# Optimization experiments

Hardware: AMD Instinct MI355X
Metric: run time of the kernel (lower is better)

Reference implementation:

```python
import jax, jax.numpy as jnp
import numpy as np

C = 512
C8 = C // 8  # reduceRate = 8


def setup_inputs() -> dict:
    key = jax.random.key(0)
    ks = jax.random.split(key, 8)
    B, H, W = 4, 64, 64
    x = jax.random.normal(ks[0], (B, C, H, W), dtype=jnp.float32)
    # 1x1 convs == per-pixel linear maps: weight [out, in], bias [out]
    sb = 1.0 / np.sqrt(C)
    Wb = jax.random.uniform(ks[1], (C8, C), jnp.float32, -sb, sb)
    bb = jax.random.uniform(ks[2], (C8,), jnp.float32, -sb, sb)
    Wc = jax.random.uniform(ks[3], (C8, C), jnp.float32, -sb, sb)
    bc = jax.random.uniform(ks[4], (C8,), jnp.float32, -sb, sb)
    Wd = jax.random.uniform(ks[5], (C, C), jnp.float32, -sb, sb)
    bd = jax.random.uniform(ks[6], (C,), jnp.float32, -sb, sb)
    # nn.Parameter(torch.zeros(1)) -> use small nonzero so grads are nontrivial
    alpha = jnp.full((1,), 0.1, dtype=jnp.float32)
    return {"x": x, "Wb": Wb, "bb": bb, "Wc": Wc, "bc": bc,
            "Wd": Wd, "bd": bd, "alpha": alpha}


def reference(x, Wb, bb, Wc, bc, Wd, bd, alpha):
    B, Cin, H, W = x.shape
    N = H * W
    xf = x.reshape(B, Cin, N)                                    # [B,C,N]
    feat_b = jnp.einsum('oc,bcn->bon', Wb, xf) + bb[None, :, None]  # [B,C/8,N]
    feat_c = jnp.einsum('oc,bcn->bon', Wc, xf) + bc[None, :, None]  # [B,C/8,N]
    # attention_s[b,n,m] = softmax_m( b^T c ), unscaled as in source
    attn = jax.nn.softmax(jnp.einsum('bkn,bkm->bnm', feat_b, feat_c), axis=-1)
    feat_d = jnp.einsum('oc,bcn->bon', Wd, xf) + bd[None, :, None]  # [B,C,N]
    # feat_e = feat_d @ attn^T : e[b,c,n] = sum_m d[b,c,m] * attn[b,n,m]
    feat_e = jnp.einsum('bcm,bnm->bcn', feat_d, attn)
    out = (alpha[0] * feat_e).reshape(B, Cin, H, W) + x
    return out
```

## Files before the change

### kernel.cpp

```cpp
#include <hip/hip_runtime.h>
#include <hip/hip_bf16.h>
#include <math.h>

#define BB 4
#define CC 512
#define NN 4096
#define LOG2E 1.4426950408889634f

typedef short short8 __attribute__((ext_vector_type(8)));
typedef float f32x4 __attribute__((ext_vector_type(4)));
typedef float f32x16 __attribute__((ext_vector_type(16)));
typedef unsigned int u32x2 __attribute__((ext_vector_type(2)));

#define MFMA16(a, b, c) __builtin_amdgcn_mfma_f32_16x16x32_bf16((a), (b), (c), 0, 0, 0)
#define MFMA32(a, b, c) __builtin_amdgcn_mfma_f32_32x32x16_bf16((a), (b), (c), 0, 0, 0)

static __device__ __forceinline__ unsigned short f2bf(float f) {
    union { float f; unsigned int u; } v; v.f = f;
    unsigned int r = v.u + 0x7FFFu + ((v.u >> 16) & 1u);
    return (unsigned short)(r >> 16);
}

static __device__ __forceinline__ unsigned int pk2bf(float a, float b) {
    __hip_bfloat162 t = __float22bfloat162_rn(make_float2(a, b));
    return *(unsigned int*)&t;
}

static __device__ __forceinline__ void gload16(const void* g, void* l) {
    __builtin_amdgcn_global_load_lds(
        (const __attribute__((address_space(1))) unsigned int*)g,
        (__attribute__((address_space(3))) unsigned int*)l, 16, 0, 0);
}

__global__ __launch_bounds__(256) void k_wconv(
    const float* __restrict__ Wb, const float* __restrict__ bb,
    const float* __restrict__ Wc, const float* __restrict__ bc,
    const float* __restrict__ Wd, const float* __restrict__ bd,
    unsigned short* __restrict__ Wcat, float* __restrict__ bcat)
{
    int r = blockIdx.x;
    int t = threadIdx.x;
    const float* src; const float* bsrc; int bi; float scale;
    if (r < 64)       { src = Wb + (size_t)r * 512;         bsrc = bb; bi = r;       scale = LOG2E; }
    else if (r < 128) { src = Wc + (size_t)(r - 64) * 512;  bsrc = bc; bi = r - 64;  scale = 1.0f; }
    else              { src = Wd + (size_t)(r - 128) * 512; bsrc = bd; bi = r - 128; scale = 1.0f; }
    float2 v = *(const float2*)&src[t * 2];
    *(unsigned int*)&Wcat[(size_t)r * 512 + t * 2] = pk2bf(v.x * scale, v.y * scale);
    if (t == 0) bcat[r] = bsrc[bi] * scale;
}

__global__ __launch_bounds__(256) void k_transpose(
    const float* __restrict__ x, unsigned short* __restrict__ xT)
{
    __shared__ float lds[64][65];
    int bid = blockIdx.x;
    int cb = bid & 7;
    int nb = (bid >> 3) & 63;
    int b  = bid >> 9;
    int t = threadIdx.x;
    int r = t >> 4;
    int q = t & 15;

#pragma unroll
    for (int p = 0; p < 4; ++p) {
        int c = p * 16 + r;
        const float4 v = *(const float4*)&x[((size_t)(b * CC + cb * 64 + c)) * NN + nb * 64 + q * 4];
        lds[c][q * 4 + 0] = v.x;
        lds[c][q * 4 + 1] = v.y;
        lds[c][q * 4 + 2] = v.z;
        lds[c][q * 4 + 3] = v.w;
    }
    __syncthreads();
#pragma unroll
    for (int p = 0; p < 4; ++p) {
        int n = p * 16 + r;
        ushort4 o;
        o.x = f2bf(lds[q * 4 + 0][n]);
        o.y = f2bf(lds[q * 4 + 1][n]);
        o.z = f2bf(lds[q * 4 + 2][n]);
        o.w = f2bf(lds[q * 4 + 3][n]);
        *(ushort4*)&xT[((size_t)(b * NN + nb * 64 + n)) * CC + cb * 64 + q * 4] = o;
    }
}

__global__ __launch_bounds__(256) void k_feat(
    const unsigned short* __restrict__ xT,
    const unsigned short* __restrict__ Wcat,
    const float* __restrict__ bcat,
    unsigned short* __restrict__ Q,
    unsigned short* __restrict__ Kf,
    unsigned short* __restrict__ Vtl)
{
    int bid = blockIdx.x;
    int ob = bid % 10;
    int nb = (bid / 10) & 63;
    int b  = bid / 640;
    int t = threadIdx.x, w = t >> 6, lane = t & 63;
    int lr = lane & 15, lg = lane >> 4;

    int o_local = w * 16 + lr;
    int wr = (ob == 0) ? o_local : (ob == 1 ? 64 + o_local : 128 + (ob - 2) * 64 + o_local);
    const unsigned short* Wrow = Wcat + (size_t)wr * CC;
    const unsigned short* xrow = xT + ((size_t)(b * NN + nb * 64)) * CC;

    f32x4 acc[4] = {};

    for (int kt = 0; kt < 8; ++kt) {
        int k0 = kt * 64;
        short8 bfr[2];
#pragma unroll
        for (int ks = 0; ks < 2; ++ks)
            bfr[ks] = *(const short8*)&Wrow[k0 + ks * 32 + lg * 8];
#pragma unroll
        for (int rf = 0; rf < 4; ++rf) {
#pragma unroll
            for (int ks = 0; ks < 2; ++ks) {
                short8 a = *(const short8*)&xrow[(size_t)(rf * 16 + lr) * CC + k0 + ks * 32 + lg * 8];
                acc[rf] = MFMA16(a, bfr[ks], acc[rf]);
            }
        }
    }

    float bias = bcat[wr];
#pragma unroll
    for (int rf = 0; rf < 4; ++rf) {
        if (ob < 2) {
            unsigned short* dst = (ob == 0) ? Q : Kf;
#pragma unroll
            for (int i = 0; i < 4; ++i) {
                int n = nb * 64 + rf * 16 + lg * 4 + i;
                dst[((size_t)(b * NN + n)) * 64 + o_local] = f2bf(acc[rf][i] + bias);
            }
        } else {
            int row = (ob - 2) * 64 + o_local;
            int nl = rf * 16 + lg * 4;
            ushort4 o4;
            o4.x = f2bf(acc[rf][0] + bias);
            o4.y = f2bf(acc[rf][1] + bias);
            o4.z = f2bf(acc[rf][2] + bias);
            o4.w = f2bf(acc[rf][3] + bias);
            *(ushort4*)&Vtl[(((size_t)(b * 64 + nb)) * CC + row) * 64 + nl] = o4;
        }
    }
}

__global__ __launch_bounds__(512, 1) void k_attn(
    const unsigned short* __restrict__ Q,
    const unsigned short* __restrict__ Kf,
    const unsigned short* __restrict__ Vtl,
    const float* __restrict__ x,
    const float* __restrict__ alpha_p,
    float* __restrict__ out)
{
    __shared__ __align__(16) unsigned short Klds[2][64 * 64];
    __shared__ __align__(16) unsigned short Vlds[2][256 * 64];
    __shared__ __align__(16) unsigned short Plds[128 * 64];
    __shared__ float Lacc[2][128];

    int bid0 = blockIdx.x;
    int bid = ((bid0 & 7) << 5) | (bid0 >> 3);
    int cb = bid & 1;
    int qb = (bid >> 1) & 31;
    int b  = bid >> 6;
    int tid = threadIdx.x;
    int w = tid >> 6, lane = tid & 63;
    int l31 = lane & 31, h = lane >> 5;
    int qi = w >> 1, mi = w & 1;

    const char* Kbase = (const char*)Kf + (size_t)b * NN * 128;
    const char* Vbase = (const char*)Vtl + (((size_t)b * 64) * CC + (size_t)cb * 256) * 128;

    short8 qfr[4];
    {
        const unsigned short* qp = Q + ((size_t)(b * NN) + qb * 128 + qi * 32 + l31) * 64;
#pragma unroll
        for (int kk = 0; kk < 4; ++kk)
            qfr[kk] = *(const short8*)&qp[kk * 16 + h * 8];
    }

    int pb[4];
#pragma unroll
    for (int kk = 0; kk < 4; ++kk)
        pb[kk] = (l31 * 128 + kk * 32 + h * 16) ^ ((l31 & 7) << 4);
    int pwa[4];
#pragma unroll
    for (int j = 0; j < 4; ++j)
        pwa[j] = (l31 * 128 + mi * 64 + j * 16 + h * 8) ^ ((l31 & 7) << 4);

#define STAGE(T, BUF)                                                          \
    do {                                                                       \
        const char* ks_ = Kbase + (size_t)(T) * 8192;                          \
        const char* vs_ = Vbase + (size_t)(T) * 65536;                         \
        {                                                                      \
            int du_ = w * 1024;                                                \
            int dl_ = du_ + lane * 16;                                         \
            int sl_ = dl_ ^ (((dl_ >> 7) & 7) << 4);                           \
            gload16(ks_ + sl_, (char*)&Klds[BUF][0] + du_);                    \
        }                                                                      \
        _Pragma("unroll")                                                      \
        for (int i_ = 0; i_ < 4; ++i_) {                                       \
            int du_ = i_ * 8192 + w * 1024;                                    \
            int dl_ = du_ + lane * 16;                                         \
            int sl_ = dl_ ^ (((dl_ >> 7) & 7) << 4);                           \
            gload16(vs_ + sl_, (char*)&Vlds[BUF][0] + du_);                    \
        }                                                                      \
    } while (0)

    f32x16 acc[4] = {};
    float lsum = 0.f;

    STAGE(0, 0);
    asm volatile("s_waitcnt vmcnt(0)" ::: "memory");
    asm volatile("s_barrier" ::: "memory");

#pragma unroll 1
    for (int t = 0; t < 64; ++t) {
        int buf = t & 1;
        if (t < 63) STAGE(t + 1, buf ^ 1);

        const char* kb = (const char*)&Klds[buf][0] + mi * 4096;
        short8 kfr[4];
#pragma unroll
        for (int kk = 0; kk < 4; ++kk)
            kfr[kk] = *(const short8*)(kb + pb[kk]);

        f32x16 st = {};
        __builtin_amdgcn_s_setprio(1);
#pragma unroll
        for (int kk = 0; kk < 4; ++kk)
            st = MFMA32(kfr[kk], qfr[kk], st);
        __builtin_amdgcn_s_setprio(0);

        unsigned int pw[8];
#pragma unroll
        for (int e2 = 0; e2 < 8; ++e2) {
            float p0 = __builtin_amdgcn_exp2f(st[e2 * 2]);
            float p1 = __builtin_amdgcn_exp2f(st[e2 * 2 + 1]);
            lsum += p0 + p1;
            pw[e2] = pk2bf(p0, p1);
        }
        {
            char* pwb = (char*)&Plds[0] + qi * 4096;
#pragma unroll
            for (int j = 0; j < 4; ++j)
                *(u32x2*)(pwb + pwa[j]) = (u32x2){pw[j * 2], pw[j * 2 + 1]};
        }
        asm volatile("s_waitcnt lgkmcnt(0)" ::: "memory");
        asm volatile("s_barrier" ::: "memory");

        const char* vb = (const char*)&Vlds[buf][0] + w * 4096;
        short8 vfr[4];
#pragma unroll
        for (int kk = 0; kk < 4; ++kk)
            vfr[kk] = *(const short8*)(vb + pb[kk]);
        __builtin_amdgcn_s_setprio(1);
#pragma unroll
        for (int kk = 0; kk < 4; ++kk) {
#pragma unroll
            for (int qf = 0; qf < 4; ++qf) {
                short8 pa = *(const short8*)((const char*)&Plds[0] + qf * 4096 + pb[kk]);
                acc[qf] = MFMA32(pa, vfr[kk], acc[qf]);
            }
        }
        __builtin_amdgcn_s_setprio(0);
        asm volatile("s_waitcnt vmcnt(0)" ::: "memory");
        asm volatile("s_barrier" ::: "memory");
    }

    lsum += __shfl_xor(lsum, 32);
    if (h == 0) Lacc[mi][qi * 32 + l31] = lsum;
    __syncthreads();

    float alpha = alpha_p[0];
    int c = cb * 256 + w * 32 + l31;
#pragma unroll
    for (int qf = 0; qf < 4; ++qf) {
#pragma unroll
        for (int rg = 0; rg < 4; ++rg) {
            int nl = qf * 32 + rg * 8 + h * 4;
            float4 l0 = *(const float4*)&Lacc[0][nl];
            float4 l1 = *(const float4*)&Lacc[1][nl];
            float4 inv;
            inv.x = alpha / (l0.x + l1.x);
            inv.y = alpha / (l0.y + l1.y);
            inv.z = alpha / (l0.z + l1.z);
            inv.w = alpha / (l0.w + l1.w);
            size_t off = ((size_t)(b * CC + c)) * NN + qb * 128 + nl;
            float4 xv = *(const float4*)&x[off];
            float4 ov;
            ov.x = xv.x + acc[qf][rg * 4 + 0] * inv.x;
            ov.y = xv.y + acc[qf][rg * 4 + 1] * inv.y;
            ov.z = xv.z + acc[qf][rg * 4 + 2] * inv.z;
            ov.w = xv.w + acc[qf][rg * 4 + 3] * inv.w;
            *(float4*)&out[off] = ov;
        }
    }
#undef STAGE
}

extern "C" void kernel_launch(void* const* d_in, const int* in_sizes, int n_in,
                              void* d_out, int out_size, void* d_ws, size_t ws_size,
                              hipStream_t stream)
{
    const float* x     = (const float*)d_in[0];
    const float* Wb    = (const float*)d_in[1];
    const float* bbias = (const float*)d_in[2];
    const float* Wc    = (const float*)d_in[3];
    const float* cbias = (const float*)d_in[4];
    const float* Wd    = (const float*)d_in[5];
    const float* dbias = (const float*)d_in[6];
    const float* alpha = (const float*)d_in[7];
    float* out = (float*)d_out;

    unsigned short* xT   = (unsigned short*)d_ws;
    unsigned short* Qd   = xT + (size_t)BB * NN * CC;
    unsigned short* Kd   = Qd + (size_t)BB * NN * 64;
    unsigned short* Vtl  = Kd + (size_t)BB * NN * 64;
    unsigned short* Wcat = Vtl + (size_t)BB * NN * CC;
    float*          bcat = (float*)(Wcat + (size_t)640 * 512);

    k_wconv<<<640, 256, 0, stream>>>(Wb, bbias, Wc, cbias, Wd, dbias, Wcat, bcat);
    k_transpose<<<2048, 256, 0, stream>>>(x, xT);
    k_feat<<<2560, 256, 0, stream>>>(xT, Wcat, bcat, Qd, Kd, Vtl);
    k_attn<<<256, 512, 0, stream>>>(Qd, Kd, Vtl, x, alpha, out);
}
```

Measured before the change: 304.5 us.

## Restructure attention kernel: register-resident P via lane shuffles, split-K over keys

The attention kernel moves from 512-thread blocks over 128 queries to 256-thread blocks over 64 queries, launching 512 blocks with two blocks per CU. The P tile no longer round-trips through LDS. Probabilities are rearranged into MFMA operand layout with cross-half lane shuffles, and K fragments are loaded straight from global memory into registers, double-buffered. Each wave pair splits the key dimension and accumulates all 256 channels, then reduces through LDS at the end, which removes a mid-iteration barrier. The cost is more accumulator registers (8 f32x16 tiles) and scalar, less coalesced output stores in the epilogue.

```diff
diff --git a/kernel.cpp b/kernel.cpp
--- a/kernel.cpp
+++ b/kernel.cpp
@@ -10,7 +10,6 @@
 typedef short short8 __attribute__((ext_vector_type(8)));
 typedef float f32x4 __attribute__((ext_vector_type(4)));
 typedef float f32x16 __attribute__((ext_vector_type(16)));
-typedef unsigned int u32x2 __attribute__((ext_vector_type(2)));
 
 #define MFMA16(a, b, c) __builtin_amdgcn_mfma_f32_16x16x32_bf16((a), (b), (c), 0, 0, 0)
 #define MFMA32(a, b, c) __builtin_amdgcn_mfma_f32_32x32x16_bf16((a), (b), (c), 0, 0, 0)
@@ -144,7 +143,7 @@
     }
 }
 
-__global__ __launch_bounds__(512, 1) void k_attn(
+__global__ __launch_bounds__(256, 2) void k_attn(
     const unsigned short* __restrict__ Q,
     const unsigned short* __restrict__ Kf,
     const unsigned short* __restrict__ Vtl,
@@ -152,149 +151,153 @@
     const float* __restrict__ alpha_p,
     float* __restrict__ out)
 {
-    __shared__ __align__(16) unsigned short Klds[2][64 * 64];
-    __shared__ __align__(16) unsigned short Vlds[2][256 * 64];
-    __shared__ __align__(16) unsigned short Plds[128 * 64];
-    __shared__ float Lacc[2][128];
+    __shared__ __align__(16) char smem[2][32768];
+    __shared__ float Lacc[2][64];
 
     int bid0 = blockIdx.x;
-    int bid = ((bid0 & 7) << 5) | (bid0 >> 3);
+    int bid = (bid0 & 7) * 64 + (bid0 >> 3);
     int cb = bid & 1;
-    int qb = (bid >> 1) & 31;
-    int b  = bid >> 6;
+    int qb = (bid >> 1) & 63;
+    int b  = bid >> 7;
     int tid = threadIdx.x;
     int w = tid >> 6, lane = tid & 63;
     int l31 = lane & 31, h = lane >> 5;
     int qi = w >> 1, mi = w & 1;
 
-    const char* Kbase = (const char*)Kf + (size_t)b * NN * 128;
-    const char* Vbase = (const char*)Vtl + (((size_t)b * 64) * CC + (size_t)cb * 256) * 128;
+    const char* Vb = (const char*)Vtl + (size_t)b * (64 * 65536) + (size_t)cb * 32768;
+    const unsigned short* Kb = Kf + (size_t)b * NN * 64;
 
     short8 qfr[4];
     {
-        const unsigned short* qp = Q + ((size_t)(b * NN) + qb * 128 + qi * 32 + l31) * 64;
+        const unsigned short* qp = Q + ((size_t)b * NN + qb * 64 + qi * 32 + l31) * 64;
 #pragma unroll
         for (int kk = 0; kk < 4; ++kk)
             qfr[kk] = *(const short8*)&qp[kk * 16 + h * 8];
     }
 
-    int pb[4];
-#pragma unroll
-    for (int kk = 0; kk < 4; ++kk)
-        pb[kk] = (l31 * 128 + kk * 32 + h * 16) ^ ((l31 & 7) << 4);
-    int pwa[4];
-#pragma unroll
-    for (int j = 0; j < 4; ++j)
-        pwa[j] = (l31 * 128 + mi * 64 + j * 16 + h * 8) ^ ((l31 & 7) << 4);
+    int vbase[2];
+#pragma unroll
+    for (int kk = 0; kk < 2; ++kk)
+        vbase[kk] = (l31 * 128 + mi * 64 + kk * 32 + h * 16) ^ ((l31 & 7) << 4);
 
 #define STAGE(T, BUF)                                                          \
     do {                                                                       \
-        const char* ks_ = Kbase + (size_t)(T) * 8192;                          \
-        const char* vs_ = Vbase + (size_t)(T) * 65536;                         \
-        {                                                                      \
-            int du_ = w * 1024;                                                \
+        const char* vs_ = Vb + (size_t)(T) * 65536;                            \
+        _Pragma("unroll")                                                      \
+        for (int i_ = 0; i_ < 8; ++i_) {                                       \
+            int du_ = (i_ * 4 + w) * 1024;                                     \
             int dl_ = du_ + lane * 16;                                         \
             int sl_ = dl_ ^ (((dl_ >> 7) & 7) << 4);                           \
-            gload16(ks_ + sl_, (char*)&Klds[BUF][0] + du_);                    \
-        }                                                                      \
-        _Pragma("unroll")                                                      \
-        for (int i_ = 0; i_ < 4; ++i_) {                                       \
-            int du_ = i_ * 8192 + w * 1024;                                    \
-            int dl_ = du_ + lane * 16;                                         \
-            int sl_ = dl_ ^ (((dl_ >> 7) & 7) << 4);                           \
-            gload16(vs_ + sl_, (char*)&Vlds[BUF][0] + du_);                    \
+            gload16(vs_ + sl_, &smem[BUF][0] + du_);                           \
         }                                                                      \
     } while (0)
 
-    f32x16 acc[4] = {};
+#define KLOAD(DST, T)                                                          \
+    do {                                                                       \
+        const unsigned short* kp_ = Kb + ((size_t)(T) * 64 + mi * 32 + l31) * 64; \
+        _Pragma("unroll")                                                      \
+        for (int kk_ = 0; kk_ < 4; ++kk_)                                      \
+            DST[kk_] = *(const short8*)&kp_[kk_ * 16 + h * 8];                 \
+    } while (0)
+
+    f32x16 acc[8] = {};
     float lsum = 0.f;
+    short8 kfA[4], kfB[4];
 
     STAGE(0, 0);
+    KLOAD(kfA, 0);
     asm volatile("s_waitcnt vmcnt(0)" ::: "memory");
-    asm volatile("s_barrier" ::: "memory");
+    __builtin_amdgcn_s_barrier();
+
+#define BODY(T, BUF, KF)                                                       \
+    do {                                                                       \
+        f32x16 st = {};                                                        \
+        __builtin_amdgcn_s_setprio(1);                                         \
+        _Pragma("unroll")                                                      \
+        for (int kk = 0; kk < 4; ++kk)                                         \
+            st = MFMA32(KF[kk], qfr[kk], st);                                  \
+        __builtin_amdgcn_s_setprio(0);                                         \
+        float p[16];                                                           \
+        _Pragma("unroll")                                                      \
+        for (int e = 0; e < 16; ++e) {                                         \
+            p[e] = __builtin_amdgcn_exp2f(st[e]);                              \
+            lsum += p[e];                                                      \
+        }                                                                      \
+        unsigned int pk[4][2];                                                 \
+        _Pragma("unroll")                                                      \
+        for (int tt = 0; tt < 4; ++tt)                                         \
+            _Pragma("unroll")                                                  \
+            for (int pp = 0; pp < 2; ++pp)                                     \
+                pk[tt][pp] = pk2bf(p[4 * tt + 2 * pp], p[4 * tt + 2 * pp + 1]);\
+        short8 pfrag[2];                                                       \
+        _Pragma("unroll")                                                      \
+        for (int kk = 0; kk < 2; ++kk) {                                       \
+            unsigned int sel0 = h ? pk[2 * kk][0] : pk[2 * kk + 1][0];         \
+            unsigned int sel1 = h ? pk[2 * kk][1] : pk[2 * kk + 1][1];         \
+            unsigned int r0 = __shfl_xor(sel0, 32);                            \
+            unsigned int r1 = __shfl_xor(sel1, 32);                            \
+            union { unsigned int u[4]; short8 s; } pa;                         \
+            pa.u[0] = h ? r0 : pk[2 * kk][0];                                  \
+            pa.u[1] = h ? r1 : pk[2 * kk][1];                                  \
+            pa.u[2] = h ? pk[2 * kk + 1][0] : r0;                              \
+            pa.u[3] = h ? pk[2 * kk + 1][1] : r1;                              \
+            pfrag[kk] = pa.s;                                                  \
+        }                                                                      \
+        const char* vb_ = &smem[BUF][0];                                       \
+        __builtin_amdgcn_s_setprio(1);                                         \
+        _Pragma("unroll")                                                      \
+        for (int ct = 0; ct < 8; ++ct) {                                       \
+            short8 vf0 = *(const short8*)(vb_ + ct * 4096 + vbase[0]);         \
+            short8 vf1 = *(const short8*)(vb_ + ct * 4096 + vbase[1]);         \
+            acc[ct] = MFMA32(vf0, pfrag[0], acc[ct]);                          \
+            acc[ct] = MFMA32(vf1, pfrag[1], acc[ct]);                          \
+        }                                                                      \
+        __builtin_amdgcn_s_setprio(0);                                         \
+        asm volatile("s_waitcnt vmcnt(0)" ::: "memory");                       \
+        __builtin_amdgcn_s_barrier();                                          \
+    } while (0)
 
 #pragma unroll 1
-    for (int t = 0; t < 64; ++t) {
-        int buf = t & 1;
-        if (t < 63) STAGE(t + 1, buf ^ 1);
-
-        const char* kb = (const char*)&Klds[buf][0] + mi * 4096;
-        short8 kfr[4];
-#pragma unroll
-        for (int kk = 0; kk < 4; ++kk)
-            kfr[kk] = *(const short8*)(kb + pb[kk]);
-
-        f32x16 st = {};
-        __builtin_amdgcn_s_setprio(1);
-#pragma unroll
-        for (int kk = 0; kk < 4; ++kk)
-            st = MFMA32(kfr[kk], qfr[kk], st);
-        __builtin_amdgcn_s_setprio(0);
-
-        unsigned int pw[8];
-#pragma unroll
-        for (int e2 = 0; e2 < 8; ++e2) {
-            float p0 = __builtin_amdgcn_exp2f(st[e2 * 2]);
-            float p1 = __builtin_amdgcn_exp2f(st[e2 * 2 + 1]);
-            lsum += p0 + p1;
-            pw[e2] = pk2bf(p0, p1);
-        }
-        {
-            char* pwb = (char*)&Plds[0] + qi * 4096;
-#pragma unroll
-            for (int j = 0; j < 4; ++j)
-                *(u32x2*)(pwb + pwa[j]) = (u32x2){pw[j * 2], pw[j * 2 + 1]};
-        }
-        asm volatile("s_waitcnt lgkmcnt(0)" ::: "memory");
-        asm volatile("s_barrier" ::: "memory");
-
-        const char* vb = (const char*)&Vlds[buf][0] + w * 4096;
-        short8 vfr[4];
-#pragma unroll
-        for (int kk = 0; kk < 4; ++kk)
-            vfr[kk] = *(const short8*)(vb + pb[kk]);
-        __builtin_amdgcn_s_setprio(1);
-#pragma unroll
-        for (int kk = 0; kk < 4; ++kk) {
-#pragma unroll
-            for (int qf = 0; qf < 4; ++qf) {
-                short8 pa = *(const short8*)((const char*)&Plds[0] + qf * 4096 + pb[kk]);
-                acc[qf] = MFMA32(pa, vfr[kk], acc[qf]);
-            }
-        }
-        __builtin_amdgcn_s_setprio(0);
-        asm volatile("s_waitcnt vmcnt(0)" ::: "memory");
-        asm volatile("s_barrier" ::: "memory");
+    for (int t2 = 0; t2 < 32; ++t2) {
+        int t0 = t2 * 2;
+        STAGE(t0 + 1, 1);
+        KLOAD(kfB, t0 + 1);
+        BODY(t0, 0, kfA);
+        int nt = (t0 + 2 < 64) ? t0 + 2 : 63;
+        STAGE(nt, 0);
+        KLOAD(kfA, nt);
+        BODY(t0 + 1, 1, kfB);
     }
 
     lsum += __shfl_xor(lsum, 32);
     if (h == 0) Lacc[mi][qi * 32 + l31] = lsum;
     __syncthreads();
 
+    float* red = (float*)&smem[0][0];
+    {
+        int region = qi * 2 + (1 - mi);
+#pragma unroll
+        for (int c2 = 0; c2 < 4; ++c2)
+            *(f32x16*)(red + region * 4096 + c2 * 1024 + lane * 16) = acc[(1 - mi) * 4 + c2];
+    }
+    __syncthreads();
+
     float alpha = alpha_p[0];
-    int c = cb * 256 + w * 32 + l31;
-#pragma unroll
-    for (int qf = 0; qf < 4; ++qf) {
-#pragma unroll
-        for (int rg = 0; rg < 4; ++rg) {
-            int nl = qf * 32 + rg * 8 + h * 4;
-            float4 l0 = *(const float4*)&Lacc[0][nl];
-            float4 l1 = *(const float4*)&Lacc[1][nl];
-            float4 inv;
-            inv.x = alpha / (l0.x + l1.x);
-            inv.y = alpha / (l0.y + l1.y);
-            inv.z = alpha / (l0.z + l1.z);
-            inv.w = alpha / (l0.w + l1.w);
-            size_t off = ((size_t)(b * CC + c)) * NN + qb * 128 + nl;
-            float4 xv = *(const float4*)&x[off];
-            float4 ov;
-            ov.x = xv.x + acc[qf][rg * 4 + 0] * inv.x;
-            ov.y = xv.y + acc[qf][rg * 4 + 1] * inv.y;
-            ov.z = xv.z + acc[qf][rg * 4 + 2] * inv.z;
-            ov.w = xv.w + acc[qf][rg * 4 + 3] * inv.w;
-            *(float4*)&out[off] = ov;
+    float inv = alpha / (Lacc[0][qi * 32 + l31] + Lacc[1][qi * 32 + l31]);
+    int myreg = qi * 2 + mi;
+#pragma unroll
+    for (int c2 = 0; c2 < 4; ++c2) {
+        f32x16 o = acc[mi * 4 + c2] + *(const f32x16*)(red + myreg * 4096 + c2 * 1024 + lane * 16);
+        int cbase = cb * 256 + (mi * 4 + c2) * 32;
+#pragma unroll
+        for (int r = 0; r < 16; ++r) {
+            int row = cbase + (r & 3) + 8 * (r >> 2) + 4 * h;
+            size_t off = ((size_t)(b * CC + row)) * NN + qb * 64 + qi * 32 + l31;
+            out[off] = x[off] + o[r] * inv;
         }
     }
+#undef BODY
+#undef KLOAD
 #undef STAGE
 }
 
@@ -322,5 +325,5 @@
     k_wconv<<<640, 256, 0, stream>>>(Wb, bbias, Wc, cbias, Wd, dbias, Wcat, bcat);
     k_transpose<<<2048, 256, 0, stream>>>(x, xT);
     k_feat<<<2560, 256, 0, stream>>>(xT, Wcat, bcat, Qd, Kd, Vtl);
-    k_attn<<<256, 512, 0, stream>>>(Qd, Kd, Vtl, x, alpha, out);
-}
+    k_attn<<<512, 256, 0, stream>>>(Qd, Kd, Vtl, x, alpha, out);
+}
```

Result: slower. 334.7 us (+9.9%).
